# Performance work log

Hardware: AMD Instinct MI355X
Metric: run time of the kernel (lower is better)

Reference implementation:

```python
import jax, jax.numpy as jnp
import numpy as np

HEADS = 8
FEATURE = 512
COMPUTE = 256
SEQ = 512
BATCH = 64


def setup_inputs() -> dict:
    key = jax.random.key(0)
    ks = jax.random.split(key, 10)
    d1 = jax.random.normal(ks[0], (BATCH, FEATURE), dtype=jnp.float32)
    d2 = jax.random.normal(ks[1], (SEQ, BATCH, FEATURE), dtype=jnp.float32)
    # linear1: Linear(FEATURE -> COMPUTE) + ReLU
    w1 = jax.random.normal(ks[2], (FEATURE, COMPUTE), dtype=jnp.float32) * (1.0 / np.sqrt(FEATURE))
    b1 = jnp.zeros((COMPUTE,), dtype=jnp.float32)
    # per-head score params, stacked: ws[i] is [2C, C], ps[i] is [C, 1]
    W = jax.random.normal(ks[3], (HEADS, 2 * COMPUTE, COMPUTE), dtype=jnp.float32)
    P = jax.random.normal(ks[4], (HEADS, COMPUTE), dtype=jnp.float32)
    # value projection weight_v: [FEATURE, COMPUTE]
    wv = jax.random.normal(ks[5], (FEATURE, COMPUTE), dtype=jnp.float32)
    # cc: Linear(COMPUTE*HEADS -> 128) + ReLU
    wcc = jax.random.normal(ks[6], (COMPUTE * HEADS, 128), dtype=jnp.float32) * (1.0 / np.sqrt(COMPUTE * HEADS))
    bcc = jnp.zeros((128,), dtype=jnp.float32)
    return {"d1": d1, "d2": d2, "w1": w1, "b1": b1, "W": W, "P": P,
            "wv": wv, "wcc": wcc, "bcc": bcc, "d2_size": SEQ}


def reference(d1, d2, w1, b1, W, P, wv, wcc, bcc, d2_size):
    S, B, F = d2.shape
    # linear1 on flattened d2 rows -> [S*B, C]
    d3 = jax.nn.relu(d2.reshape(-1, F) @ w1 + b1)
    # linear1 on d1, tiled S times along batch axis -> [S*B, C]
    d4 = jax.nn.relu(d1 @ w1 + b1)            # [B, C]
    d4 = jnp.tile(d4, (S, 1))                  # [S*B, C]
    d5 = jnp.concatenate([d3, d4], axis=1).reshape(S, B, -1)  # [S, B, 2C]
    # value path: tanh(d2 @ weight_v) -> [B, S, C]
    tv = jnp.tanh(jnp.einsum('sbf,fc->sbc', d2, wv)).transpose(1, 0, 2)
    # all heads batched: us = tanh(d5 @ W_h) -> [H, S, B, C]
    us = jnp.tanh(jnp.einsum('sbd,hdc->hsbc', d5, W))
    atts = jnp.einsum('hsbc,hc->hbs', us, P)   # [H, B, S]
    scores = jax.nn.softmax(atts, axis=-1)     # softmax over sequence
    vs = jnp.einsum('hbs,bsc->hbc', scores, tv)  # weighted sum over S -> [H, B, C]
    # torch.cat(vs, dim=1): head-major concat -> [B, H*C]
    vs = vs.transpose(1, 0, 2).reshape(B, -1)
    return jax.nn.relu(vs @ wcc + bcc)         # [B, 128]
```

## Files before the change

kernel.cpp:

```cpp
#include <hip/hip_runtime.h>
#include <cstddef>
#include <cstdint>

#define HH 8
#define FF 512
#define CC 256
#define SS 512
#define BB 64
#define SB (SS*BB)

typedef __attribute__((ext_vector_type(4))) float f32x4;
typedef __attribute__((ext_vector_type(8))) short bf16x8;

typedef __attribute__((address_space(1))) unsigned int gu32_t;
typedef __attribute__((address_space(3))) unsigned int lu32_t;

__device__ __forceinline__ void gld16(const void* gp, void* lp) {
    __builtin_amdgcn_global_load_lds((gu32_t*)gp, (lu32_t*)lp, 16, 0, 0);
}

__device__ __forceinline__ float fast_tanh(float x) {
    float e = __expf(2.0f * x);
    return 1.0f - 2.0f / (e + 1.0f);
}
__device__ __forceinline__ float relu_f(float x) { return fmaxf(x, 0.0f); }

__device__ __forceinline__ unsigned short f2bf(float x) {
    unsigned u = __float_as_uint(x);
    unsigned r = u + 0x7FFFu + ((u >> 16) & 1u);
    return (unsigned short)(r >> 16);
}
__device__ __forceinline__ float bf2f(unsigned short h) {
    return __uint_as_float(((unsigned)h) << 16);
}


__global__ __launch_bounds__(256) void p_prep(
    const float* __restrict__ w1, const float* __restrict__ wv,
    const float* __restrict__ W, const float* __restrict__ d1,
    const float* __restrict__ b1,
    unsigned short* __restrict__ w1ts, unsigned short* __restrict__ wvts,
    unsigned short* __restrict__ Wts, float* __restrict__ d4)
{
    __shared__ float T[64][65];
    __shared__ float As[16][68];
    __shared__ float Bs[16][68];
    const int tid = threadIdx.x;
    const int bid = blockIdx.x;
    if (bid < 192) {
        const float* src;
        unsigned short* dst;
        int kt64, nt;
        if (bid < 64) {
            int m = bid >> 5;
            int t = bid & 31;
            kt64 = t >> 2; nt = t & 3;
            src = m ? wv : w1;
            dst = m ? wvts : w1ts;
        } else {
            int t = bid - 64;
            int h = t >> 4; int tt = t & 15;
            kt64 = tt >> 2; nt = tt & 3;
            src = W + (size_t)h * 2 * CC * CC;
            dst = Wts + (size_t)h * 8 * CC * 64;
        }
        const int k0 = kt64 * 64, n0 = nt * 64;
        #pragma unroll
        for (int jj = 0; jj < 4; ++jj) {
            int i = (tid >> 4) + jj * 16;
            int j = (tid & 15) * 4;
            float4 v = *(const float4*)(src + (size_t)(k0 + i) * CC + n0 + j);
            T[i][j] = v.x; T[i][j+1] = v.y; T[i][j+2] = v.z; T[i][j+3] = v.w;
        }
        __syncthreads();
        {
            const int n_local = tid & 63;
            const int kg = (tid >> 6) * 16;
            const int n_abs = n0 + n_local;
            const int sxn = n_abs & 7;
            #pragma unroll
            for (int j = 0; j < 2; ++j) {
                const int kbase = kg + j * 8;
                const int k_abs = k0 + kbase;
                const int kt = k_abs >> 5;
                const int g = (k_abs >> 3) & 3;
                bf16x8 hv8, lv8;
                #pragma unroll
                for (int q = 0; q < 8; ++q) {
                    float x = T[kbase + q][n_local];
                    unsigned short hx = f2bf(x);
                    hv8[q] = (short)hx;
                    lv8[q] = (short)f2bf(x - bf2f(hx));
                }
                size_t rowo = ((size_t)kt * CC + n_abs) * 64;
                *(bf16x8*)(dst + rowo + (size_t)((2*g + 0) ^ sxn) * 8) = hv8;
                *(bf16x8*)(dst + rowo + (size_t)((2*g + 1) ^ sxn) * 8) = lv8;
            }
        }
    } else {
        const int n0 = (bid - 192) * 64;
        const int tx = tid & 15, ty = tid >> 4;
        const int lm = tid >> 2, lk4 = (tid & 3) * 4;
        const int bk = tid >> 4, bn4 = (tid & 15) * 4;
        float acc[4][4] = {};
        for (int k0 = 0; k0 < FF; k0 += 16) {
            float4 a = *(const float4*)(d1 + (size_t)lm * FF + k0 + lk4);
            As[lk4+0][lm] = a.x; As[lk4+1][lm] = a.y;
            As[lk4+2][lm] = a.z; As[lk4+3][lm] = a.w;
            *(float4*)&Bs[bk][bn4] = *(const float4*)(w1 + (size_t)(k0+bk)*CC + n0 + bn4);
            __syncthreads();
            #pragma unroll
            for (int kk = 0; kk < 16; ++kk) {
                float4 a4 = *(const float4*)&As[kk][ty*4];
                float4 b4 = *(const float4*)&Bs[kk][tx*4];
                float av[4] = {a4.x, a4.y, a4.z, a4.w};
                float bv[4] = {b4.x, b4.y, b4.z, b4.w};
                #pragma unroll
                for (int i = 0; i < 4; ++i)
                    #pragma unroll
                    for (int j = 0; j < 4; ++j)
                        acc[i][j] = fmaf(av[i], bv[j], acc[i][j]);
            }
            __syncthreads();
        }
        #pragma unroll
        for (int i = 0; i < 4; ++i) {
            int row = ty*4 + i;
            #pragma unroll
            for (int j = 0; j < 4; ++j)
                d4[(size_t)row*CC + n0 + tx*4 + j] = relu_f(acc[i][j] + b1[n0 + tx*4 + j]);
        }
    }
}

__global__ __launch_bounds__(256, 2) void k1_main(
    const float* __restrict__ d2,
    const unsigned short* __restrict__ w1ts, const unsigned short* __restrict__ wvts,
    const float* __restrict__ b1,
    const float* __restrict__ d4, const float* __restrict__ W,
    unsigned short* __restrict__ d3s, unsigned short* __restrict__ tv,
    float* __restrict__ e4)
{
    __shared__ __align__(16) unsigned short SH[24576];
    unsigned short* const Abuf = SH;
    unsigned short* const Bbuf = SH + 8192;

    const int tid = threadIdx.x;
    const int bid = blockIdx.x;

    if (bid >= 512) {
        float (*As)[68] = (float(*)[68])&SH[0];
        float (*Bs)[68] = (float(*)[68])&SH[8192];
        const int idx = bid - 512;
        const int n0 = (idx & 3) * 64;
        const int h  = idx >> 2;
        const float* Wh = W + ((size_t)h * 2 * CC + CC) * CC;
        const int tx = tid & 15, ty = tid >> 4;
        const int lm = tid >> 2, lk4 = (tid & 3) * 4;
        const int bk = tid >> 4, bn4 = (tid & 15) * 4;
        float acc[4][4] = {};
        for (int k0 = 0; k0 < CC; k0 += 16) {
            float4 a = *(const float4*)(d4 + (size_t)lm * CC + k0 + lk4);
            As[lk4+0][lm] = a.x; As[lk4+1][lm] = a.y;
            As[lk4+2][lm] = a.z; As[lk4+3][lm] = a.w;
            *(float4*)&Bs[bk][bn4] = *(const float4*)(Wh + (size_t)(k0+bk)*CC + n0 + bn4);
            __syncthreads();
            #pragma unroll
            for (int kk = 0; kk < 16; ++kk) {
                float4 a4 = *(const float4*)&As[kk][ty*4];
                float4 b4 = *(const float4*)&Bs[kk][tx*4];
                float av[4] = {a4.x, a4.y, a4.z, a4.w};
                float bv[4] = {b4.x, b4.y, b4.z, b4.w};
                #pragma unroll
                for (int i = 0; i < 4; ++i)
                    #pragma unroll
                    for (int j = 0; j < 4; ++j)
                        acc[i][j] = fmaf(av[i], bv[j], acc[i][j]);
            }
            __syncthreads();
        }
        #pragma unroll
        for (int i = 0; i < 4; ++i) {
            int b = ty*4 + i;
            #pragma unroll
            for (int j = 0; j < 4; ++j)
                e4[((size_t)h*BB + b)*CC + n0 + tx*4 + j] = acc[i][j];
        }
        return;
    }

    const int cxcd = bid & 7;
    const int jd   = bid >> 3;
    const int path = jd & 1;
    const int xb   = (jd >> 1) * 8 + cxcd;
    const int r0   = xb * 128;
    const int lane = tid & 63, w = tid >> 6;
    const int rowgrp = w & 1, colgrp = w >> 1;
    const int cb = lane & 15, quad = lane >> 4;
    const unsigned short* BT = path ? wvts : w1ts;

    f32x4 acc[4][8];
    f32x4 zero = {0.0f, 0.0f, 0.0f, 0.0f};
    #pragma unroll
    for (int rt = 0; rt < 4; ++rt)
        #pragma unroll
        for (int ct = 0; ct < 8; ++ct) acc[rt][ct] = zero;

    const int ar = tid >> 1, ak = (tid & 1) * 16;
    const int arx = ar & 7;
    const int g0 = ak >> 3;
    const int phi = (2 * quad) ^ (cb & 7);

    for (int k0 = 0; k0 < FF; k0 += 32) {
        const int kt = k0 >> 5;
        {
            const unsigned short* Bsrc = BT + (size_t)kt * (CC * 64);
            #pragma unroll
            for (int i = 0; i < 8; ++i) {
                int chunk = i * 4 + w;
                gld16(Bsrc + (size_t)chunk * 512 + lane * 8, &Bbuf[chunk * 512]);
            }
        }
        {
            const float* s = d2 + (size_t)(r0 + ar) * FF + k0 + ak;
            float v[16];
            *(float4*)&v[0]  = *(const float4*)(s);
            *(float4*)&v[4]  = *(const float4*)(s + 4);
            *(float4*)&v[8]  = *(const float4*)(s + 8);
            *(float4*)&v[12] = *(const float4*)(s + 12);
            bf16x8 vh0, vh1, vl0, vl1;
            #pragma unroll
            for (int j = 0; j < 8; ++j) {
                unsigned short h = f2bf(v[j]);
                vh0[j] = (short)h; vl0[j] = (short)f2bf(v[j] - bf2f(h));
                unsigned short h2 = f2bf(v[j+8]);
                vh1[j] = (short)h2; vl1[j] = (short)f2bf(v[j+8] - bf2f(h2));
            }
            unsigned short* Ar = &Abuf[ar * 64];
            *(bf16x8*)&Ar[((2*g0 + 0) ^ arx) * 8] = vh0;
            *(bf16x8*)&Ar[((2*g0 + 1) ^ arx) * 8] = vl0;
            *(bf16x8*)&Ar[((2*g0 + 2) ^ arx) * 8] = vh1;
            *(bf16x8*)&Ar[((2*g0 + 3) ^ arx) * 8] = vl1;
        }
        __syncthreads();
        bf16x8 ahf[4], alf[4];
        #pragma unroll
        for (int rt = 0; rt < 4; ++rt) {
            const unsigned short* Arow = &Abuf[(rowgrp*64 + rt*16 + cb) * 64];
            ahf[rt] = *(const bf16x8*)&Arow[phi * 8];
            alf[rt] = *(const bf16x8*)&Arow[(phi ^ 1) * 8];
        }
        #pragma unroll
        for (int ct = 0; ct < 8; ++ct) {
            const unsigned short* Brow = &Bbuf[(colgrp*128 + ct*16 + cb) * 64];
            bf16x8 bh = *(const bf16x8*)&Brow[phi * 8];
            bf16x8 bl = *(const bf16x8*)&Brow[(phi ^ 1) * 8];
            #pragma unroll
            for (int rt = 0; rt < 4; ++rt) {
                acc[rt][ct] = __builtin_amdgcn_mfma_f32_16x16x32_bf16(ahf[rt], bh, acc[rt][ct], 0, 0, 0);
                acc[rt][ct] = __builtin_amdgcn_mfma_f32_16x16x32_bf16(ahf[rt], bl, acc[rt][ct], 0, 0, 0);
                acc[rt][ct] = __builtin_amdgcn_mfma_f32_16x16x32_bf16(alf[rt], bh, acc[rt][ct], 0, 0, 0);
            }
        }
        __syncthreads();
    }

    if (path == 0) {
        float bias[8];
        #pragma unroll
        for (int ct = 0; ct < 8; ++ct) bias[ct] = b1[colgrp*128 + ct*16 + cb];
        unsigned short* Lp = SH + colgrp * 9216;
        #pragma unroll
        for (int it = 0; it < 4; ++it) {
            __syncthreads();
            #pragma unroll
            for (int rt = 0; rt < 4; ++rt)
                #pragma unroll
                for (int r = 0; r < 4; ++r) {
                    int row = rowgrp*64 + rt*16 + quad*4 + r;
                    int sx = row & 7;
                    #pragma unroll
                    for (int t = 0; t < 2; ++t) {
                        float val = relu_f(acc[rt][2*it + t][r] + bias[2*it + t]);
                        unsigned short hx = f2bf(val);
                        unsigned short lx = f2bf(val - bf2f(hx));
                        int cl = t*16 + cb;
                        int g = cl >> 3, c7 = cl & 7;
                        Lp[row*72 + (((2*g + 0) ^ sx) << 3) + c7] = hx;
                        Lp[row*72 + (((2*g + 1) ^ sx) << 3) + c7] = lx;
                    }
                }
            __syncthreads();
            #pragma unroll
            for (int q = 0; q < 8; ++q) {
                int idx = q*256 + tid;
                int pp  = idx >> 10;
                int rc  = idx & 1023;
                int row = rc >> 3;
                int ch  = rc & 7;
                bf16x8 v = *(const bf16x8*)&SH[pp*9216 + row*72 + ch*8];
                unsigned short* dst = d3s + ((size_t)(pp*4 + it) * SB + r0 + row) * 64;
                *(bf16x8*)&dst[ch*8] = v;
            }
        }
    } else {
        unsigned short* Lp = SH + colgrp * 6144;
        #pragma unroll
        for (int it = 0; it < 4; ++it) {
            __syncthreads();
            #pragma unroll
            for (int rt = 0; rt < 4; ++rt)
                #pragma unroll
                for (int r = 0; r < 4; ++r) {
                    int row = rowgrp*64 + rt*16 + quad*4 + r;
                    #pragma unroll
                    for (int t = 0; t < 2; ++t) {
                        int cl = t*16 + cb;
                        Lp[row*48 + cl] = f2bf(fast_tanh(acc[rt][2*it + t][r]));
                    }
                }
            __syncthreads();
            #pragma unroll
            for (int q = 0; q < 4; ++q) {
                int idx = q*256 + tid;
                int pp  = idx >> 9;
                int rc  = idx & 511;
                int row = rc >> 2;
                int ch  = rc & 3;
                bf16x8 v = *(const bf16x8*)&SH[pp*6144 + row*48 + ch*8];
                unsigned short* dst = tv + (size_t)(r0 + row) * CC + (pp*4 + it)*32;
                *(bf16x8*)&dst[ch*8] = v;
            }
        }
    }
}

__global__ __launch_bounds__(256, 2) void k3_atts(
    const unsigned short* __restrict__ d3s, const unsigned short* __restrict__ Wts,
    const float* __restrict__ e4, const float* __restrict__ P,
    float* __restrict__ atts)
{
    __shared__ __align__(16) unsigned short Abuf[128 * 64];
    __shared__ __align__(16) unsigned short Bbuf[256 * 64];
    float (*red)[128] = (float(*)[128])&Abuf[0];

    const int tid = threadIdx.x;
    const int lane = tid & 63, w = tid >> 6;
    const int bid = blockIdx.x;
    const int cxcd = bid & 7;
    const int jj   = bid >> 3;
    const int h    = jj & 7;
    const int xb   = (jj >> 3) * 8 + cxcd;
    const int r0   = xb * 128;
    const int rowgrp = w & 1, colgrp = w >> 1;
    const int cb = lane & 15, quad = lane >> 4;
    const int phi = (2 * quad) ^ (cb & 7);

    const unsigned short* Wh = Wts + (size_t)h * (8 * CC * 64);

    f32x4 acc[4][8];
    f32x4 zero = {0.0f, 0.0f, 0.0f, 0.0f};
    #pragma unroll
    for (int rt = 0; rt < 4; ++rt)
        #pragma unroll
        for (int ct = 0; ct < 8; ++ct) acc[rt][ct] = zero;

    for (int kt = 0; kt < 8; ++kt) {
        {
            const unsigned short* Asrc = d3s + ((size_t)kt * SB + r0) * 64;
            #pragma unroll
            for (int i = 0; i < 4; ++i) {
                int chunk = i * 4 + w;
                gld16(Asrc + (size_t)chunk * 512 + lane * 8, &Abuf[chunk * 512]);
            }
        }
        {
            const unsigned short* Bsrc = Wh + (size_t)kt * (CC * 64);
            #pragma unroll
            for (int i = 0; i < 8; ++i) {
                int chunk = i * 4 + w;
                gld16(Bsrc + (size_t)chunk * 512 + lane * 8, &Bbuf[chunk * 512]);
            }
        }
        __syncthreads();
        bf16x8 ahf[4], alf[4];
        #pragma unroll
        for (int rt = 0; rt < 4; ++rt) {
            const unsigned short* Arow = &Abuf[(rowgrp*64 + rt*16 + cb) * 64];
            ahf[rt] = *(const bf16x8*)&Arow[phi * 8];
            alf[rt] = *(const bf16x8*)&Arow[(phi ^ 1) * 8];
        }
        #pragma unroll
        for (int ct = 0; ct < 8; ++ct) {
            const unsigned short* Brow = &Bbuf[(colgrp*128 + ct*16 + cb) * 64];
            bf16x8 bh = *(const bf16x8*)&Brow[phi * 8];
            bf16x8 bl = *(const bf16x8*)&Brow[(phi ^ 1) * 8];
            #pragma unroll
            for (int rt = 0; rt < 4; ++rt) {
                acc[rt][ct] = __builtin_amdgcn_mfma_f32_16x16x32_bf16(ahf[rt], bh, acc[rt][ct], 0, 0, 0);
                acc[rt][ct] = __builtin_amdgcn_mfma_f32_16x16x32_bf16(ahf[rt], bl, acc[rt][ct], 0, 0, 0);
                acc[rt][ct] = __builtin_amdgcn_mfma_f32_16x16x32_bf16(alf[rt], bh, acc[rt][ct], 0, 0, 0);
            }
        }
        __syncthreads();
    }
    float Pv[8];
    #pragma unroll
    for (int ct = 0; ct < 8; ++ct) Pv[ct] = P[(size_t)h * CC + colgrp*128 + ct*16 + cb];
    #pragma unroll
    for (int rt = 0; rt < 4; ++rt) {
        #pragma unroll
        for (int r = 0; r < 4; ++r) {
            int b = rt*16 + quad*4 + r;
            const float* e4p = e4 + ((size_t)h * BB + b) * CC + colgrp*128 + cb;
            float part = 0.0f;
            #pragma unroll
            for (int ct = 0; ct < 8; ++ct) {
                float u = acc[rt][ct][r] + e4p[ct*16];
                part = fmaf(Pv[ct], fast_tanh(u), part);
            }
            part += __shfl_xor(part, 1); part += __shfl_xor(part, 2);
            part += __shfl_xor(part, 4); part += __shfl_xor(part, 8);
            if (cb == 0) red[colgrp][rowgrp*64 + b] = part;
        }
    }
    __syncthreads();
    if (tid < 128) {
        float v = red[0][tid] + red[1][tid];
        int gr = r0 + tid;
        int s = gr >> 6, b = gr & 63;
        atts[((size_t)h * BB + b) * SS + s] = v;
    }
}

__global__ __launch_bounds__(256) void k456a(
    const float* __restrict__ atts, const unsigned short* __restrict__ tv,
    float* __restrict__ vsp)
{
    __shared__ float sc[HH][SS];
    __shared__ float red[4][2048];
    const int bq = blockIdx.x;
    const int b = bq >> 2, q = bq & 3;
    const int tid = threadIdx.x;
    const int lane = tid & 63, w = tid >> 6;

    for (int i = tid; i < HH*SS; i += 256) {
        int h = i >> 9, s = i & 511;
        sc[h][s] = atts[((size_t)h*BB + b)*SS + s];
    }
    __syncthreads();
    #pragma unroll
    for (int t = 0; t < 2; ++t) {
        int hh = w*2 + t;
        float x[8];
        #pragma unroll
        for (int j = 0; j < 8; ++j) x[j] = sc[hh][j*64 + lane];
        float m = x[0];
        #pragma unroll
        for (int j = 1; j < 8; ++j) m = fmaxf(m, x[j]);
        #pragma unroll
        for (int d = 1; d < 64; d <<= 1) m = fmaxf(m, __shfl_xor(m, d));
        float sum = 0.0f;
        #pragma unroll
        for (int j = 0; j < 8; ++j) { x[j] = __expf(x[j] - m); sum += x[j]; }
        #pragma unroll
        for (int d = 1; d < 64; d <<= 1) sum += __shfl_xor(sum, d);
        float inv = 1.0f / sum;
        #pragma unroll
        for (int j = 0; j < 8; ++j) sc[hh][j*64 + lane] = x[j] * inv;
    }
    __syncthreads();
    {
        const int c0 = lane * 4;
        const int s0 = q*128 + w*32;
        const unsigned short* tvb = tv + ((size_t)s0 * BB + b) * CC + c0;
        float acc[HH][4] = {};
        for (int si = 0; si < 32; ++si) {
            uint2 u = *(const uint2*)(tvb + (size_t)si * BB * CC);
            float x0 = bf2f((unsigned short)(u.x));
            float x1 = bf2f((unsigned short)(u.x >> 16));
            float x2 = bf2f((unsigned short)(u.y));
            float x3 = bf2f((unsigned short)(u.y >> 16));
            int s = s0 + si;
            #pragma unroll
            for (int h = 0; h < HH; ++h) {
                float wgt = sc[h][s];
                acc[h][0] = fmaf(wgt, x0, acc[h][0]);
                acc[h][1] = fmaf(wgt, x1, acc[h][1]);
                acc[h][2] = fmaf(wgt, x2, acc[h][2]);
                acc[h][3] = fmaf(wgt, x3, acc[h][3]);
            }
        }
        #pragma unroll
        for (int h = 0; h < HH; ++h)
            #pragma unroll
            for (int j = 0; j < 4; ++j)
                red[w][h*256 + c0 + j] = acc[h][j];
    }
    __syncthreads();
    float* dst = vsp + ((size_t)b * 4 + q) * 2048;
    for (int i = tid; i < 2048; i += 256)
        dst[i] = red[0][i] + red[1][i] + red[2][i] + red[3][i];
}

__global__ __launch_bounds__(256) void k456b(
    const float* __restrict__ vsp, const float* __restrict__ wcc,
    const float* __restrict__ bcc, float* __restrict__ out)
{
    __shared__ float vs[2048];
    __shared__ float tmp[256];
    const int b = blockIdx.x;
    const int tid = threadIdx.x;
    const float* src = vsp + (size_t)b * 4 * 2048;
    for (int i = tid; i < 2048; i += 256)
        vs[i] = src[i] + src[2048 + i] + src[4096 + i] + src[6144 + i];
    __syncthreads();
    {
        const int n = tid & 127, half = tid >> 7;
        float o = 0.0f;
        const int kbase = half * 1024;
        for (int k = 0; k < 1024; ++k)
            o = fmaf(vs[kbase + k], wcc[(size_t)(kbase + k) * 128 + n], o);
        tmp[half * 128 + n] = o;
    }
    __syncthreads();
    if (tid < 128)
        out[(size_t)b * 128 + tid] = relu_f(tmp[tid] + tmp[128 + tid] + bcc[tid]);
}

extern "C" void kernel_launch(void* const* d_in, const int* in_sizes, int n_in,
                              void* d_out, int out_size, void* d_ws, size_t ws_size,
                              hipStream_t stream)
{
    (void)in_sizes; (void)n_in; (void)out_size; (void)ws_size;
    const float* d1  = (const float*)d_in[0];
    const float* d2  = (const float*)d_in[1];
    const float* w1  = (const float*)d_in[2];
    const float* b1  = (const float*)d_in[3];
    const float* W   = (const float*)d_in[4];
    const float* P   = (const float*)d_in[5];
    const float* wv  = (const float*)d_in[6];
    const float* wcc = (const float*)d_in[7];
    const float* bcc = (const float*)d_in[8];
    float* out = (float*)d_out;

    char* p = (char*)d_ws;
    unsigned short* d3s  = (unsigned short*)p; p += (size_t)8 * SB * 64 * 2;
    unsigned short* tv   = (unsigned short*)p; p += (size_t)SB * CC * 2;
    unsigned short* w1ts = (unsigned short*)p; p += (size_t)16 * CC * 64 * 2;
    unsigned short* wvts = (unsigned short*)p; p += (size_t)16 * CC * 64 * 2;
    unsigned short* Wts  = (unsigned short*)p; p += (size_t)HH * 8 * CC * 64 * 2;
    float* d4   = (float*)p;  p += (size_t)BB * CC * 4;
    float* e4   = (float*)p;  p += (size_t)HH * BB * CC * 4;
    float* atts = (float*)p;  p += (size_t)HH * BB * SS * 4;
    float* vsp  = (float*)p;  p += (size_t)BB * 4 * 2048 * 4;

    p_prep   <<<dim3(196),       256, 0, stream>>>(w1, wv, W, d1, b1,
                  w1ts, wvts, Wts, d4);
    k1_main  <<<dim3(544),       256, 0, stream>>>(d2, w1ts, wvts, b1, d4, W,
                  d3s, tv, e4);
    k3_atts  <<<dim3(2048),      256, 0, stream>>>(d3s, Wts, e4, P, atts);
    k456a    <<<dim3(256),       256, 0, stream>>>(atts, tv, vsp);
    k456b    <<<dim3(BB),        256, 0, stream>>>(vsp, wcc, bcc, out);
}
```

Measured before the change: 348.7 us.

## Double-buffer weight tiles in attention-score GEMM and prefetch two steps ahead

```diff
diff --git a/kernel.cpp b/kernel.cpp
--- a/kernel.cpp
+++ b/kernel.cpp
@@ -341,7 +341,7 @@
     float* __restrict__ atts)
 {
     __shared__ __align__(16) unsigned short Abuf[128 * 64];
-    __shared__ __align__(16) unsigned short Bbuf[256 * 64];
+    __shared__ __align__(16) unsigned short Bbuf[2][256 * 64];
     float (*red)[128] = (float(*)[128])&Abuf[0];
 
     const int tid = threadIdx.x;
@@ -365,24 +365,30 @@
         #pragma unroll
         for (int ct = 0; ct < 8; ++ct) acc[rt][ct] = zero;
 
+    {
+        #pragma unroll
+        for (int i = 0; i < 8; ++i) {
+            int chunk = i * 4 + w;
+            gld16(Wh + (size_t)chunk * 512 + lane * 8, &Bbuf[0][chunk * 512]);
+        }
+        const unsigned short* Asrc = d3s + (size_t)r0 * 64;
+        #pragma unroll
+        for (int i = 0; i < 4; ++i) {
+            int chunk = i * 4 + w;
+            gld16(Asrc + (size_t)chunk * 512 + lane * 8, &Abuf[chunk * 512]);
+        }
+        const unsigned short* Bsrc1 = Wh + (size_t)(CC * 64);
+        #pragma unroll
+        for (int i = 0; i < 8; ++i) {
+            int chunk = i * 4 + w;
+            gld16(Bsrc1 + (size_t)chunk * 512 + lane * 8, &Bbuf[1][chunk * 512]);
+        }
+    }
+    asm volatile("s_waitcnt vmcnt(8)" ::: "memory");
+    __builtin_amdgcn_s_barrier();
+    __builtin_amdgcn_sched_barrier(0);
+
     for (int kt = 0; kt < 8; ++kt) {
-        {
-            const unsigned short* Asrc = d3s + ((size_t)kt * SB + r0) * 64;
-            #pragma unroll
-            for (int i = 0; i < 4; ++i) {
-                int chunk = i * 4 + w;
-                gld16(Asrc + (size_t)chunk * 512 + lane * 8, &Abuf[chunk * 512]);
-            }
-        }
-        {
-            const unsigned short* Bsrc = Wh + (size_t)kt * (CC * 64);
-            #pragma unroll
-            for (int i = 0; i < 8; ++i) {
-                int chunk = i * 4 + w;
-                gld16(Bsrc + (size_t)chunk * 512 + lane * 8, &Bbuf[chunk * 512]);
-            }
-        }
-        __syncthreads();
         bf16x8 ahf[4], alf[4];
         #pragma unroll
         for (int rt = 0; rt < 4; ++rt) {
@@ -390,9 +396,10 @@
             ahf[rt] = *(const bf16x8*)&Arow[phi * 8];
             alf[rt] = *(const bf16x8*)&Arow[(phi ^ 1) * 8];
         }
+        const unsigned short* Bb = &Bbuf[kt & 1][0];
         #pragma unroll
         for (int ct = 0; ct < 8; ++ct) {
-            const unsigned short* Brow = &Bbuf[(colgrp*128 + ct*16 + cb) * 64];
+            const unsigned short* Brow = &Bb[(colgrp*128 + ct*16 + cb) * 64];
             bf16x8 bh = *(const bf16x8*)&Brow[phi * 8];
             bf16x8 bl = *(const bf16x8*)&Brow[(phi ^ 1) * 8];
             #pragma unroll
@@ -402,7 +409,29 @@
                 acc[rt][ct] = __builtin_amdgcn_mfma_f32_16x16x32_bf16(alf[rt], bh, acc[rt][ct], 0, 0, 0);
             }
         }
-        __syncthreads();
+        __builtin_amdgcn_s_barrier();
+        __builtin_amdgcn_sched_barrier(0);
+        if (kt < 7) {
+            const unsigned short* Asrc = d3s + ((size_t)(kt + 1) * SB + r0) * 64;
+            #pragma unroll
+            for (int i = 0; i < 4; ++i) {
+                int chunk = i * 4 + w;
+                gld16(Asrc + (size_t)chunk * 512 + lane * 8, &Abuf[chunk * 512]);
+            }
+            if (kt < 6) {
+                const unsigned short* Bsrc = Wh + (size_t)(kt + 2) * (CC * 64);
+                #pragma unroll
+                for (int i = 0; i < 8; ++i) {
+                    int chunk = i * 4 + w;
+                    gld16(Bsrc + (size_t)chunk * 512 + lane * 8, &Bbuf[kt & 1][chunk * 512]);
+                }
+                asm volatile("s_waitcnt vmcnt(8)" ::: "memory");
+            } else {
+                asm volatile("s_waitcnt vmcnt(0)" ::: "memory");
+            }
+            __builtin_amdgcn_s_barrier();
+            __builtin_amdgcn_sched_barrier(0);
+        }
     }
     float Pv[8];
     #pragma unroll
```

Result: no change. 349.3 us (+0.2%).
